# Kernel tuning notes

Hardware: AMD Instinct MI355X
Metric: run time of the kernel (lower is better)

The kernel has to match this reference:

```python
import jax, jax.numpy as jnp
import numpy as np
import math

PHI = (1 + math.sqrt(5)) / 2
VOCAB = 50257
EMBED_DIM = 1024
NUM_WINDINGS = 8
EPS = 1e-5


def _generate_coprimes(n):
    coprimes = [1, 2]
    while len(coprimes) < n:
        nxt = int(coprimes[-1] * PHI) + 1
        while any(math.gcd(nxt, c) > 1 for c in coprimes):
            nxt += 1
        coprimes.append(nxt)
    return coprimes[:n]


def setup_inputs() -> dict:
    key = jax.random.key(0)
    k1, k2, k3 = jax.random.split(key, 3)
    B, S = 8, 4096
    x = jax.random.randint(k1, (B, S), 0, VOCAB, dtype=jnp.int64)
    windings = jnp.asarray(_generate_coprimes(NUM_WINDINGS), dtype=jnp.float32)
    win_dim = 2 * NUM_WINDINGS
    # nn.Linear default init: U(-1/sqrt(fan_in), 1/sqrt(fan_in))
    bound = 1.0 / math.sqrt(win_dim)
    proj_w = jax.random.uniform(k2, (EMBED_DIM, win_dim), jnp.float32, -bound, bound)
    proj_b = jax.random.uniform(k3, (EMBED_DIM,), jnp.float32, -bound, bound)
    gamma = jnp.ones((EMBED_DIM,), jnp.float32)
    beta = jnp.zeros((EMBED_DIM,), jnp.float32)
    return {"x": x, "windings": windings, "proj_w": proj_w, "proj_b": proj_b,
            "gamma": gamma, "beta": beta}


def reference(x, windings, proj_w, proj_b, gamma, beta):
    # t in [0,1): fractional position on the torus
    t = x.astype(jnp.float32) / VOCAB                      # (B, S)
    angle = (2.0 * jnp.pi) * t[..., None] * windings       # (B, S, W)
    # torch loop appends cos, sin per winding -> interleaved [cos0,sin0,cos1,sin1,...]
    feats = jnp.stack([jnp.cos(angle), jnp.sin(angle)], axis=-1)  # (B, S, W, 2)
    feats = feats.reshape(*angle.shape[:-1], 2 * windings.shape[0])  # (B, S, 2W)
    emb = jnp.einsum('bsf,df->bsd', feats, proj_w) + proj_b  # (B, S, D)
    # SyntonicNorm: LayerNorm-style normalization over embed_dim with affine params
    mu = jnp.mean(emb, axis=-1, keepdims=True)
    var = jnp.mean(jnp.square(emb - mu), axis=-1, keepdims=True)
    normed = (emb - mu) * jax.lax.rsqrt(var + EPS)
    return normed * gamma + beta
```

## Files before the change

kernel.cpp:

```cpp
#include <hip/hip_runtime.h>
#include <math.h>


#define TWO_PI 6.28318530717958647692f
#define INV_VOCAB (1.0f / 50257.0f)
#define INV_D (1.0f / 1024.0f)
#define ROWS_PB 32
#define PSTRIDE 320
#define FINAL_OFF 20480

typedef float f32x4 __attribute__((ext_vector_type(4)));

__global__ __launch_bounds__(256) void stats_partial(const float* __restrict__ pw,
                                                     const float* __restrict__ pb,
                                                     float* __restrict__ ws) {
  const int t = threadIdx.x;
  const int b = blockIdx.x;
  const int f = t >> 4, g = t & 15;
  const int d0 = b * 16;

  float m = 0.f, mw = 0.f, cc = 0.f, b1 = 0.f, b2 = 0.f;
#pragma unroll
  for (int k = 0; k < 16; ++k) {
    const int d = d0 + k;
    const float wf = pw[d * 16 + f];
    const float wg = pw[d * 16 + g];
    m = fmaf(wf, wg, m);
    if (g == 0) {
      const float bb = pb[d];
      mw += wf;
      cc = fmaf(wf, bb, cc);
      if (f == 0) {
        b1 += bb;
        b2 = fmaf(bb, bb, b2);
      }
    }
  }
  float* p = ws + b * PSTRIDE;
  p[t] = m * INV_D;
  if (g == 0) {
    p[256 + f] = mw * INV_D;
    p[272 + f] = cc * INV_D;
    if (f == 0) {
      p[288] = b1 * INV_D;
      p[289] = b2 * INV_D;
    }
  }
}

__global__ __launch_bounds__(320) void stats_reduce(float* __restrict__ ws) {
  const int t = threadIdx.x;
  float s = 0.f;
#pragma unroll
  for (int b = 0; b < 64; ++b) s += ws[b * PSTRIDE + t];
  ws[FINAL_OFF + t] = s;
}

__global__ __launch_bounds__(256) void wind_main(const int* __restrict__ x,
                                                 const float* __restrict__ winds,
                                                 const float* __restrict__ pw,
                                                 const float* __restrict__ pb,
                                                 const float* __restrict__ gamma,
                                                 const float* __restrict__ beta,
                                                 const float* __restrict__ ws,
                                                 float* __restrict__ out) {
  __shared__ __align__(16) float feat[ROWS_PB][20];
  __shared__ __align__(16) float Mlds[16][20];
  __shared__ float mwl[16], cl[16], cst[2];
  __shared__ float murs[ROWS_PB][2];

  const int tid = threadIdx.x;
  const int d = blockIdx.x * 256 + tid;
  const int row0 = blockIdx.y * ROWS_PB;

  Mlds[tid >> 4][tid & 15] = ws[tid];
  if (tid < 16) mwl[tid] = ws[256 + tid];
  else if (tid < 32) cl[tid - 16] = ws[272 + tid - 16];
  else if (tid < 34) cst[tid - 32] = ws[288 + tid - 32];

  const f32x4 w0 = reinterpret_cast<const f32x4*>(pw)[d * 4 + 0];
  const f32x4 w1 = reinterpret_cast<const f32x4*>(pw)[d * 4 + 1];
  const f32x4 w2 = reinterpret_cast<const f32x4*>(pw)[d * 4 + 2];
  const f32x4 w3 = reinterpret_cast<const f32x4*>(pw)[d * 4 + 3];
  const float pbd = pb[d];
  const float gd = gamma[d];
  const float bd = beta[d];

#pragma unroll
  for (int s = 0; s < 2; ++s) {
    const int slot = tid + s * 256;
    const int r = slot >> 4, jj = slot & 15;
    const float tf = (float)x[row0 + r] * INV_VOCAB;
    float sn, cs;
    sincosf(TWO_PI * tf * winds[jj >> 1], &sn, &cs);
    feat[r][jj] = (jj & 1) ? sn : cs;
  }
  __syncthreads();

  {
    const int jj = tid & 15;
    const float mwj = mwl[jj];
    const float cj = cl[jj];
    const f32x4 M0 = *reinterpret_cast<const f32x4*>(&Mlds[jj][0]);
    const f32x4 M1 = *reinterpret_cast<const f32x4*>(&Mlds[jj][4]);
    const f32x4 M2 = *reinterpret_cast<const f32x4*>(&Mlds[jj][8]);
    const f32x4 M3 = *reinterpret_cast<const f32x4*>(&Mlds[jj][12]);
#pragma unroll
    for (int h = 0; h < 2; ++h) {
      const int r = (tid >> 4) + h * 16;
      const f32x4 F0 = *reinterpret_cast<const f32x4*>(&feat[r][0]);
      const f32x4 F1 = *reinterpret_cast<const f32x4*>(&feat[r][4]);
      const f32x4 F2 = *reinterpret_cast<const f32x4*>(&feat[r][8]);
      const f32x4 F3 = *reinterpret_cast<const f32x4*>(&feat[r][12]);
      float acc = 0.f;
      acc = fmaf(M0.x, F0.x, acc); acc = fmaf(M0.y, F0.y, acc);
      acc = fmaf(M0.z, F0.z, acc); acc = fmaf(M0.w, F0.w, acc);
      acc = fmaf(M1.x, F1.x, acc); acc = fmaf(M1.y, F1.y, acc);
      acc = fmaf(M1.z, F1.z, acc); acc = fmaf(M1.w, F1.w, acc);
      acc = fmaf(M2.x, F2.x, acc); acc = fmaf(M2.y, F2.y, acc);
      acc = fmaf(M2.z, F2.z, acc); acc = fmaf(M2.w, F2.w, acc);
      acc = fmaf(M3.x, F3.x, acc); acc = fmaf(M3.y, F3.y, acc);
      acc = fmaf(M3.z, F3.z, acc); acc = fmaf(M3.w, F3.w, acc);
      const float fjj = feat[r][jj];
      float pE = fjj * fmaf(2.f, cj, acc);
      float pM = fjj * mwj;
#pragma unroll
      for (int off = 1; off < 16; off <<= 1) {
        pE += __shfl_xor(pE, off);
        pM += __shfl_xor(pM, off);
      }
      if (jj == 0) {
        const float mu = pM + cst[0];
        const float var = (pE + cst[1]) - mu * mu;
        murs[r][0] = mu;
        murs[r][1] = rsqrtf(var + 1e-5f);
      }
    }
  }
  __syncthreads();

  float* o = out + (size_t)row0 * 1024 + d;
#pragma unroll 2
  for (int r = 0; r < ROWS_PB; ++r) {
    const f32x4 F0 = *reinterpret_cast<const f32x4*>(&feat[r][0]);
    const f32x4 F1 = *reinterpret_cast<const f32x4*>(&feat[r][4]);
    const f32x4 F2 = *reinterpret_cast<const f32x4*>(&feat[r][8]);
    const f32x4 F3 = *reinterpret_cast<const f32x4*>(&feat[r][12]);
    float e = pbd;
    e = fmaf(w0.x, F0.x, e); e = fmaf(w0.y, F0.y, e);
    e = fmaf(w0.z, F0.z, e); e = fmaf(w0.w, F0.w, e);
    e = fmaf(w1.x, F1.x, e); e = fmaf(w1.y, F1.y, e);
    e = fmaf(w1.z, F1.z, e); e = fmaf(w1.w, F1.w, e);
    e = fmaf(w2.x, F2.x, e); e = fmaf(w2.y, F2.y, e);
    e = fmaf(w2.z, F2.z, e); e = fmaf(w2.w, F2.w, e);
    e = fmaf(w3.x, F3.x, e); e = fmaf(w3.y, F3.y, e);
    e = fmaf(w3.z, F3.z, e); e = fmaf(w3.w, F3.w, e);
    const float mu = murs[r][0];
    const float rs = murs[r][1];
    const float a = rs * gd;
    o[(size_t)r * 1024] = fmaf(e, a, fmaf(-mu, a, bd));
  }
}

extern "C" void kernel_launch(void* const* d_in, const int* in_sizes, int n_in,
                              void* d_out, int out_size, void* d_ws, size_t ws_size,
                              hipStream_t stream) {
  const int* x = (const int*)d_in[0];
  const float* winds = (const float*)d_in[1];
  const float* pw = (const float*)d_in[2];
  const float* pb = (const float*)d_in[3];
  const float* gamma = (const float*)d_in[4];
  const float* beta = (const float*)d_in[5];
  float* out = (float*)d_out;
  float* ws = (float*)d_ws;

  const int rows = in_sizes[0];
  stats_partial<<<64, 256, 0, stream>>>(pw, pb, ws);
  stats_reduce<<<1, 320, 0, stream>>>(ws);
  dim3 grid(4, (unsigned)(rows / ROWS_PB));
  wind_main<<<grid, 256, 0, stream>>>(x, winds, pw, pb, gamma, beta,
                                      ws + FINAL_OFF, out);
}
```

Before: 42.20 us.

## Fuse stats reduction into partial kernel via flag spin, double rows per block

Merges the two-kernel weight-statistics reduction into one kernel. Each block publishes a release flag, and block 0 spins on all flags before summing the partials and then resets the flags. This removes one kernel launch from the stream. The change also doubles rows per block in the main kernel, amortising per-block setup and weight loads, and makes output stores nontemporal. The spin-wait assumes all 64 blocks are co-resident, which holds for this small grid, and relies on flag memory starting at zero or being reset after each call.

```diff
diff --git a/kernel.cpp b/kernel.cpp
--- a/kernel.cpp
+++ b/kernel.cpp
@@ -5,15 +5,18 @@
 #define TWO_PI 6.28318530717958647692f
 #define INV_VOCAB (1.0f / 50257.0f)
 #define INV_D (1.0f / 1024.0f)
-#define ROWS_PB 32
+#define ROWS_PB 64
 #define PSTRIDE 320
+#define NPART 64
 #define FINAL_OFF 20480
+#define FLAG_OFF 20800
+#define FLAG_MAGIC 0x5A5A5A5Au
 
 typedef float f32x4 __attribute__((ext_vector_type(4)));
 
-__global__ __launch_bounds__(256) void stats_partial(const float* __restrict__ pw,
-                                                     const float* __restrict__ pb,
-                                                     float* __restrict__ ws) {
+__global__ __launch_bounds__(256) void stats_all(const float* __restrict__ pw,
+                                                 const float* __restrict__ pb,
+                                                 float* __restrict__ ws) {
   const int t = threadIdx.x;
   const int b = blockIdx.x;
   const int f = t >> 4, g = t & 15;
@@ -46,14 +49,36 @@
       p[289] = b2 * INV_D;
     }
   }
-}
-
-__global__ __launch_bounds__(320) void stats_reduce(float* __restrict__ ws) {
-  const int t = threadIdx.x;
-  float s = 0.f;
-#pragma unroll
-  for (int b = 0; b < 64; ++b) s += ws[b * PSTRIDE + t];
-  ws[FINAL_OFF + t] = s;
+
+  unsigned* flags = reinterpret_cast<unsigned*>(ws) + FLAG_OFF;
+  __syncthreads();
+  __threadfence();
+  if (t == 0)
+    __hip_atomic_store(&flags[b], FLAG_MAGIC, __ATOMIC_RELEASE,
+                       __HIP_MEMORY_SCOPE_AGENT);
+
+  if (b == 0) {
+    if (t < NPART) {
+      while (__hip_atomic_load(&flags[t], __ATOMIC_ACQUIRE,
+                               __HIP_MEMORY_SCOPE_AGENT) != FLAG_MAGIC) {
+      }
+    }
+    __syncthreads();
+    __threadfence();
+    float s = 0.f;
+#pragma unroll
+    for (int bb = 0; bb < NPART; ++bb) s += ws[bb * PSTRIDE + t];
+    ws[FINAL_OFF + t] = s;
+    if (t < 34) {
+      float s2 = 0.f;
+#pragma unroll
+      for (int bb = 0; bb < NPART; ++bb) s2 += ws[bb * PSTRIDE + 256 + t];
+      ws[FINAL_OFF + 256 + t] = s2;
+    }
+    __syncthreads();
+    if (t < NPART) flags[t] = 0u;
+    __threadfence();
+  }
 }
 
 __global__ __launch_bounds__(256) void wind_main(const int* __restrict__ x,
@@ -73,10 +98,10 @@
   const int d = blockIdx.x * 256 + tid;
   const int row0 = blockIdx.y * ROWS_PB;
 
-  Mlds[tid >> 4][tid & 15] = ws[tid];
-  if (tid < 16) mwl[tid] = ws[256 + tid];
-  else if (tid < 32) cl[tid - 16] = ws[272 + tid - 16];
-  else if (tid < 34) cst[tid - 32] = ws[288 + tid - 32];
+  Mlds[tid >> 4][tid & 15] = ws[FINAL_OFF + tid];
+  if (tid < 16) mwl[tid] = ws[FINAL_OFF + 256 + tid];
+  else if (tid < 32) cl[tid - 16] = ws[FINAL_OFF + 256 + tid - 16 + 16];
+  else if (tid < 34) cst[tid - 32] = ws[FINAL_OFF + 256 + tid];
 
   const f32x4 w0 = reinterpret_cast<const f32x4*>(pw)[d * 4 + 0];
   const f32x4 w1 = reinterpret_cast<const f32x4*>(pw)[d * 4 + 1];
@@ -87,7 +112,7 @@
   const float bd = beta[d];
 
 #pragma unroll
-  for (int s = 0; s < 2; ++s) {
+  for (int s = 0; s < 4; ++s) {
     const int slot = tid + s * 256;
     const int r = slot >> 4, jj = slot & 15;
     const float tf = (float)x[row0 + r] * INV_VOCAB;
@@ -106,7 +131,7 @@
     const f32x4 M2 = *reinterpret_cast<const f32x4*>(&Mlds[jj][8]);
     const f32x4 M3 = *reinterpret_cast<const f32x4*>(&Mlds[jj][12]);
 #pragma unroll
-    for (int h = 0; h < 2; ++h) {
+    for (int h = 0; h < 4; ++h) {
       const int r = (tid >> 4) + h * 16;
       const f32x4 F0 = *reinterpret_cast<const f32x4*>(&feat[r][0]);
       const f32x4 F1 = *reinterpret_cast<const f32x4*>(&feat[r][4]);
@@ -158,7 +183,8 @@
     const float mu = murs[r][0];
     const float rs = murs[r][1];
     const float a = rs * gd;
-    o[(size_t)r * 1024] = fmaf(e, a, fmaf(-mu, a, bd));
+    __builtin_nontemporal_store(fmaf(e, a, fmaf(-mu, a, bd)),
+                                o + (size_t)r * 1024);
   }
 }
 
@@ -175,9 +201,7 @@
   float* ws = (float*)d_ws;
 
   const int rows = in_sizes[0];
-  stats_partial<<<64, 256, 0, stream>>>(pw, pb, ws);
-  stats_reduce<<<1, 320, 0, stream>>>(ws);
+  stats_all<<<NPART, 256, 0, stream>>>(pw, pb, ws);
   dim3 grid(4, (unsigned)(rows / ROWS_PB));
-  wind_main<<<grid, 256, 0, stream>>>(x, winds, pw, pb, gamma, beta,
-                                      ws + FINAL_OFF, out);
+  wind_main<<<grid, 256, 0, stream>>>(x, winds, pw, pb, gamma, beta, ws, out);
 }
```

Result: slower. 52.08 us (+23.4%).

## Have each thread cover four output columns so one block spans a full row

Applied to the files above, without the earlier changes.

Each thread now holds the projection weights for four consecutive embedding columns in registers and writes one 16-byte vector store per row. A single block therefore covers all 1024 columns of its 32 rows. The grid drops from 4x1024 to 1024 blocks, which cuts the redundant per-block sincos feature computation and the row statistics work by a factor of four. The cost is much higher register pressure (64 weight floats per thread), which can lower occupancy, and fewer blocks overall.

```diff
diff --git a/kernel.cpp b/kernel.cpp
--- a/kernel.cpp
+++ b/kernel.cpp
@@ -70,21 +70,22 @@
   __shared__ float murs[ROWS_PB][2];
 
   const int tid = threadIdx.x;
-  const int d = blockIdx.x * 256 + tid;
-  const int row0 = blockIdx.y * ROWS_PB;
+  const int row0 = blockIdx.x * ROWS_PB;
 
   Mlds[tid >> 4][tid & 15] = ws[tid];
   if (tid < 16) mwl[tid] = ws[256 + tid];
-  else if (tid < 32) cl[tid - 16] = ws[272 + tid - 16];
-  else if (tid < 34) cst[tid - 32] = ws[288 + tid - 32];
-
-  const f32x4 w0 = reinterpret_cast<const f32x4*>(pw)[d * 4 + 0];
-  const f32x4 w1 = reinterpret_cast<const f32x4*>(pw)[d * 4 + 1];
-  const f32x4 w2 = reinterpret_cast<const f32x4*>(pw)[d * 4 + 2];
-  const f32x4 w3 = reinterpret_cast<const f32x4*>(pw)[d * 4 + 3];
-  const float pbd = pb[d];
-  const float gd = gamma[d];
-  const float bd = beta[d];
+  else if (tid < 32) cl[tid - 16] = ws[256 + tid];
+  else if (tid < 34) cst[tid - 32] = ws[256 + tid];
+
+  float4 wreg[4][4];
+#pragma unroll
+  for (int r = 0; r < 4; ++r)
+#pragma unroll
+    for (int c = 0; c < 4; ++c)
+      wreg[r][c] = reinterpret_cast<const float4*>(pw)[(tid * 4 + r) * 4 + c];
+  const float4 pbv = reinterpret_cast<const float4*>(pb)[tid];
+  const float4 gv = reinterpret_cast<const float4*>(gamma)[tid];
+  const float4 bv = reinterpret_cast<const float4*>(beta)[tid];
 
 #pragma unroll
   for (int s = 0; s < 2; ++s) {
@@ -139,26 +140,44 @@
   }
   __syncthreads();
 
-  float* o = out + (size_t)row0 * 1024 + d;
+  float* o = out + (size_t)row0 * 1024 + tid * 4;
 #pragma unroll 2
   for (int r = 0; r < ROWS_PB; ++r) {
     const f32x4 F0 = *reinterpret_cast<const f32x4*>(&feat[r][0]);
     const f32x4 F1 = *reinterpret_cast<const f32x4*>(&feat[r][4]);
     const f32x4 F2 = *reinterpret_cast<const f32x4*>(&feat[r][8]);
     const f32x4 F3 = *reinterpret_cast<const f32x4*>(&feat[r][12]);
-    float e = pbd;
-    e = fmaf(w0.x, F0.x, e); e = fmaf(w0.y, F0.y, e);
-    e = fmaf(w0.z, F0.z, e); e = fmaf(w0.w, F0.w, e);
-    e = fmaf(w1.x, F1.x, e); e = fmaf(w1.y, F1.y, e);
-    e = fmaf(w1.z, F1.z, e); e = fmaf(w1.w, F1.w, e);
-    e = fmaf(w2.x, F2.x, e); e = fmaf(w2.y, F2.y, e);
-    e = fmaf(w2.z, F2.z, e); e = fmaf(w2.w, F2.w, e);
-    e = fmaf(w3.x, F3.x, e); e = fmaf(w3.y, F3.y, e);
-    e = fmaf(w3.z, F3.z, e); e = fmaf(w3.w, F3.w, e);
+    float e[4];
+#pragma unroll
+    for (int k = 0; k < 4; ++k) {
+      float a = (k == 0) ? pbv.x : (k == 1) ? pbv.y : (k == 2) ? pbv.z : pbv.w;
+      a = fmaf(wreg[k][0].x, F0.x, a);
+      a = fmaf(wreg[k][0].y, F0.y, a);
+      a = fmaf(wreg[k][0].z, F0.z, a);
+      a = fmaf(wreg[k][0].w, F0.w, a);
+      a = fmaf(wreg[k][1].x, F1.x, a);
+      a = fmaf(wreg[k][1].y, F1.y, a);
+      a = fmaf(wreg[k][1].z, F1.z, a);
+      a = fmaf(wreg[k][1].w, F1.w, a);
+      a = fmaf(wreg[k][2].x, F2.x, a);
+      a = fmaf(wreg[k][2].y, F2.y, a);
+      a = fmaf(wreg[k][2].z, F2.z, a);
+      a = fmaf(wreg[k][2].w, F2.w, a);
+      a = fmaf(wreg[k][3].x, F3.x, a);
+      a = fmaf(wreg[k][3].y, F3.y, a);
+      a = fmaf(wreg[k][3].z, F3.z, a);
+      a = fmaf(wreg[k][3].w, F3.w, a);
+      e[k] = a;
+    }
     const float mu = murs[r][0];
     const float rs = murs[r][1];
-    const float a = rs * gd;
-    o[(size_t)r * 1024] = fmaf(e, a, fmaf(-mu, a, bd));
+    const float s0 = gv.x * rs, s1 = gv.y * rs, s2 = gv.z * rs, s3 = gv.w * rs;
+    f32x4 res;
+    res.x = fmaf(e[0], s0, fmaf(-mu, s0, bv.x));
+    res.y = fmaf(e[1], s1, fmaf(-mu, s1, bv.y));
+    res.z = fmaf(e[2], s2, fmaf(-mu, s2, bv.z));
+    res.w = fmaf(e[3], s3, fmaf(-mu, s3, bv.w));
+    *reinterpret_cast<f32x4*>(o + (size_t)r * 1024) = res;
   }
 }
 
@@ -177,7 +196,6 @@
   const int rows = in_sizes[0];
   stats_partial<<<64, 256, 0, stream>>>(pw, pb, ws);
   stats_reduce<<<1, 320, 0, stream>>>(ws);
-  dim3 grid(4, (unsigned)(rows / ROWS_PB));
-  wind_main<<<grid, 256, 0, stream>>>(x, winds, pw, pb, gamma, beta,
-                                      ws + FINAL_OFF, out);
-}
+  wind_main<<<rows / ROWS_PB, 256, 0, stream>>>(x, winds, pw, pb, gamma, beta,
+                                                ws + FINAL_OFF, out);
+}
```

After: 41.01 us. 2.8% less time.
